# Kernel optimization log

Measured on AMD Instinct MI355X. Metric: run time of the kernel, lower is better.

## Reference

```python
import jax, jax.numpy as jnp
import numpy as np
import math

N_HEADS = 16
D_MODEL = 1024
M = D_MODEL // N_HEADS  # per-head dim = 64

def _kaiming_uniform(key, shape):
    # torch kaiming_uniform_ with a=sqrt(5) on [h, fan_in, fan_out]-style 3D tensor:
    # fan_in = shape[1] (size of dim 1), gain = sqrt(2/(1+a^2)) = sqrt(1/3)
    fan_in = shape[1]
    gain = math.sqrt(2.0 / (1.0 + 5.0))
    bound = gain * math.sqrt(3.0 / fan_in)
    return jax.random.uniform(key, shape, dtype=jnp.float32, minval=-bound, maxval=bound)

def setup_inputs() -> dict:
    key = jax.random.key(0)
    kx, kq, kk, kv, ko = jax.random.split(key, 5)
    x = jax.random.normal(kx, (4, 2048, D_MODEL), dtype=jnp.float32)
    W_q = _kaiming_uniform(kq, (N_HEADS, D_MODEL, M))
    W_k = _kaiming_uniform(kk, (N_HEADS, D_MODEL, M))
    W_v = _kaiming_uniform(kv, (N_HEADS, D_MODEL, M))
    W_o = _kaiming_uniform(ko, (N_HEADS, M, D_MODEL))
    return {"x": x, "W_q": W_q, "W_k": W_k, "W_v": W_v, "W_o": W_o}

def reference(x, W_q, W_k, W_v, W_o):
    # x: [b, s, d]; W_q/W_k/W_v: [h, d, m]; W_o: [h, m, d]
    q = jnp.einsum('bsd,hdm->bhsm', x, W_q)
    k = jnp.einsum('bsd,hdm->bhsm', x, W_k)
    v = jnp.einsum('bsd,hdm->bhsm', x, W_v)
    scale = 1.0 / math.sqrt(q.shape[-1])
    scores = jnp.einsum('bhsm,bhtm->bhst', q, k) * scale  # [b,h,s,s]
    attn = jax.nn.softmax(scores, axis=-1)
    ctx = jnp.einsum('bhst,bhtm->bhsm', attn, v)
    out = jnp.einsum('bhsm,hmd->bsd', ctx, W_o)  # sum over heads
    return out
```

## Files before the change

kernel.cpp:

```cpp
#include <hip/hip_runtime.h>
#include <hip/hip_bf16.h>

typedef __attribute__((ext_vector_type(8))) short short8;
typedef __attribute__((ext_vector_type(8))) _Float16 half8;
typedef __attribute__((ext_vector_type(4))) float f32x4;
typedef __attribute__((ext_vector_type(16))) float f32x16;
typedef __attribute__((ext_vector_type(4))) unsigned int uint4v;
typedef __attribute__((ext_vector_type(2))) unsigned int uint2v;

#define NB 4
#define NH 16
#define NS 2048
#define ND 1024
#define NM 64
#define R_TOT 8192
#define N_QKV 3072
#define QKV_ONE 8388608
#define SCALE_Q 0.18033688011112042f

static __device__ __forceinline__ unsigned short f2h(float f) {
    _Float16 h = (_Float16)f;
    return __builtin_bit_cast(unsigned short, h);
}
static __device__ __forceinline__ unsigned cvtpk_h(float lo, float hiv) {
    unsigned r;
    asm("v_cvt_pkrtz_f16_f32 %0, %1, %2" : "=v"(r) : "v"(lo), "v"(hiv));
    return r;
}
static __device__ __forceinline__ void gl_lds16(const unsigned short* g, unsigned short* l) {
    __builtin_amdgcn_global_load_lds((const __attribute__((address_space(1))) void*)g,
                                     (__attribute__((address_space(3))) void*)l, 16, 0, 0);
}
static __device__ __forceinline__ half8 rd_swz(const unsigned short* base, int row, int col) {
    int byte = (row << 7) + (col << 1);
    byte ^= (row & 7) << 4;
    return *(const half8*)((const char*)base + byte);
}

__global__ __launch_bounds__(256) void k_convert_x(const float* __restrict__ x,
                                                   unsigned short* __restrict__ xh) {
    int i = blockIdx.x * 256 + threadIdx.x;
    const float4* xp = (const float4*)x;
    float4 v = xp[i];
    ushort4 o;
    o.x = f2h(v.x); o.y = f2h(v.y); o.z = f2h(v.z); o.w = f2h(v.w);
    ((ushort4*)xh)[i] = o;
}

__global__ __launch_bounds__(256) void k_convert_wqkv(const float* __restrict__ Wq,
                                                      const float* __restrict__ Wk,
                                                      const float* __restrict__ Wv,
                                                      unsigned short* __restrict__ BT) {
    int i = blockIdx.x * 256 + threadIdx.x;
    int d = i & 1023;
    int n = i >> 10;
    int w = n >> 10;
    int h = (n >> 6) & 15;
    int m = n & 63;
    const float* W = (w == 0) ? Wq : ((w == 1) ? Wk : Wv);
    float v = W[((size_t)h * ND + d) * NM + m];
    if (w == 0) v *= SCALE_Q;
    BT[i] = f2h(v);
}

__global__ __launch_bounds__(256) void k_convert_wo(const float* __restrict__ Wo,
                                                    unsigned short* __restrict__ BTo) {
    int i = blockIdx.x * 256 + threadIdx.x;
    int n = i & 1023;
    int d = i >> 10;
    BTo[i] = f2h(Wo[(size_t)n * ND + d]);
}

#define QBM 256
#define QBN 192
__global__ __launch_bounds__(512, 2) void k_gemm_qkv(const unsigned short* __restrict__ A,
                                                     const unsigned short* __restrict__ BT,
                                                     unsigned short* __restrict__ qkv) {
    __shared__ unsigned short L[2][(QBM + QBN) * 64];
    int tid = threadIdx.x;
    int bx = blockIdx.x;
    int swz = (bx & 7) * 64 + (bx >> 3);
    int rt = swz & 31;
    int ct = swz >> 5;
    int r0 = rt * QBM, c0 = ct * QBN;
    int lane = tid & 63, wid = tid >> 6;
    int l15 = lane & 15, grp = lane >> 4;
    int wrow = (wid >> 2) * 128;
    int wcol = (wid & 3) * 48;

    f32x4 acc[8][3] = {};

    auto stageA = [&](int bufi, int k0) {
        #pragma unroll
        for (int r = 0; r < 4; ++r) {
            int off = r * 4096 + tid * 8;
            int row = off >> 6;
            int sch = ((off >> 3) & 7) ^ (row & 7);
            gl_lds16(A + (size_t)(r0 + row) * 1024 + k0 + sch * 8, &L[bufi][off]);
        }
    };
    auto stageB = [&](int bufi, int k0) {
        #pragma unroll
        for (int r = 0; r < 3; ++r) {
            int off = r * 4096 + tid * 8;
            int row = off >> 6;
            int sch = ((off >> 3) & 7) ^ (row & 7);
            gl_lds16(BT + (size_t)(c0 + row) * 1024 + k0 + sch * 8, &L[bufi][QBM * 64 + off]);
        }
    };

    stageA(0, 0);
    stageB(0, 0);
    asm volatile("s_waitcnt vmcnt(0)" ::: "memory");
    __builtin_amdgcn_s_barrier();

    for (int t = 0; t < 16; ++t) {
        int buf = t & 1;
        const unsigned short* As = L[buf];
        const unsigned short* Bs = L[buf] + QBM * 64;

        half8 af[8], bf[3];
        #pragma unroll
        for (int i = 0; i < 8; ++i) af[i] = rd_swz(As, wrow + i * 16 + l15, grp * 8);
        #pragma unroll
        for (int j = 0; j < 3; ++j) bf[j] = rd_swz(Bs, wcol + j * 16 + l15, grp * 8);
        if (t < 15) { stageA(buf ^ 1, (t + 1) * 64); stageB(buf ^ 1, (t + 1) * 64); }
        __builtin_amdgcn_sched_barrier(0);
        __builtin_amdgcn_s_setprio(1);
        #pragma unroll
        for (int i = 0; i < 8; ++i)
            #pragma unroll
            for (int j = 0; j < 3; ++j)
                acc[i][j] = __builtin_amdgcn_mfma_f32_16x16x32_f16(af[i], bf[j], acc[i][j], 0, 0, 0);
        __builtin_amdgcn_s_setprio(0);

        #pragma unroll
        for (int i = 0; i < 8; ++i) af[i] = rd_swz(As, wrow + i * 16 + l15, 32 + grp * 8);
        #pragma unroll
        for (int j = 0; j < 3; ++j) bf[j] = rd_swz(Bs, wcol + j * 16 + l15, 32 + grp * 8);
        __builtin_amdgcn_s_setprio(1);
        #pragma unroll
        for (int i = 0; i < 8; ++i)
            #pragma unroll
            for (int j = 0; j < 3; ++j)
                acc[i][j] = __builtin_amdgcn_mfma_f32_16x16x32_f16(af[i], bf[j], acc[i][j], 0, 0, 0);
        __builtin_amdgcn_s_setprio(0);

        asm volatile("s_waitcnt vmcnt(0)" ::: "memory");
        __builtin_amdgcn_s_barrier();
    }

    #pragma unroll
    for (int j = 0; j < 3; ++j) {
        int n_base = c0 + wcol + j * 16;
        int w = n_base >> 10;
        int nh = n_base + l15;
        int h = (nh >> 6) & 15;
        int m = nh & 63;
        if (w == 2) {
            unsigned short* outp = qkv + 2 * (size_t)QKV_ONE;
            #pragma unroll
            for (int i = 0; i < 8; ++i) {
                int rb = r0 + wrow + i * 16 + grp * 4;
                int bb = rb >> 11, s = rb & 2047;
                ushort4 pv;
                pv.x = f2h(acc[i][j][0]);
                pv.y = f2h(acc[i][j][1]);
                pv.z = f2h(acc[i][j][2]);
                pv.w = f2h(acc[i][j][3]);
                *(ushort4*)(outp + ((size_t)(bb * NH + h) * NM + m) * NS + s) = pv;
            }
        } else {
            unsigned short* outp = qkv + (size_t)w * QKV_ONE;
            #pragma unroll
            for (int i = 0; i < 8; ++i) {
                int rb = r0 + wrow + i * 16 + grp * 4;
                #pragma unroll
                for (int reg = 0; reg < 4; ++reg) {
                    int r = rb + reg;
                    int bb = r >> 11, s = r & 2047;
                    outp[((size_t)(bb * NH + h) * NS + s) * NM + m] = f2h(acc[i][j][reg]);
                }
            }
        }
    }
}

__global__ __launch_bounds__(512) void k_attn(const unsigned short* __restrict__ qkv,
                                              unsigned short* __restrict__ ctx) {
    __shared__ unsigned short Ks[2][4096];
    __shared__ unsigned short Vs[2][4096];

    int tid = threadIdx.x;
    int lane = tid & 63, wid = tid >> 6;
    int l31 = lane & 31, hi = lane >> 5;

    int bid = blockIdx.x;
    int xcd = bid & 7;
    int j = bid >> 3;
    int bh = xcd * 8 + (j >> 3);
    int qb = j & 7;
    int b = bh >> 4, h = bh & 15;

    size_t hb = (size_t)bh * NS * NM;
    const unsigned short* Qg = qkv + hb;
    const unsigned short* Kg = qkv + QKV_ONE + hb;
    const unsigned short* Vt = qkv + 2 * (size_t)QKV_ONE + hb;

    int q0 = qb * 256 + wid * 32;

    half8 qf[4];
    #pragma unroll
    for (int kk = 0; kk < 4; ++kk)
        qf[kk] = *(const half8*)(Qg + (size_t)(q0 + l31) * NM + kk * 16 + hi * 8);

    half8 ones;
    #pragma unroll
    for (int e = 0; e < 8; ++e) ones[e] = (_Float16)1.0f;

    f32x16 accO0 = {}, accO1 = {}, accS = {};

    const unsigned short* gsrc0;
    const unsigned short* gsrc1;
    unsigned short* lbase0;
    unsigned short* lbase1;
    int step0, step1;
    {
        int seg = wid * 2;
        int off = (seg & 7) * 512 + lane * 8;
        int row = off >> 6;
        int sch = ((off >> 3) & 7) ^ (row & 7);
        if (seg < 8) { gsrc0 = Kg + row * NM + sch * 8; step0 = NM;  lbase0 = &Ks[0][off]; }
        else         { gsrc0 = Vt + (size_t)row * NS + sch * 8; step0 = 1; lbase0 = &Vs[0][off]; }
        seg = wid * 2 + 1;
        off = (seg & 7) * 512 + lane * 8;
        row = off >> 6;
        sch = ((off >> 3) & 7) ^ (row & 7);
        if (seg < 8) { gsrc1 = Kg + row * NM + sch * 8; step1 = NM;  lbase1 = &Ks[0][off]; }
        else         { gsrc1 = Vt + (size_t)row * NS + sch * 8; step1 = 1; lbase1 = &Vs[0][off]; }
    }
    auto stage = [&](int bufi, int t0) {
        gl_lds16(gsrc0 + (size_t)t0 * step0, lbase0 + bufi * 4096);
        gl_lds16(gsrc1 + (size_t)t0 * step1, lbase1 + bufi * 4096);
    };

    stage(0, 0);
    stage(1, 64);

    for (int t = 0; t < 32; ++t) {
        int buf = t & 1;
        if (t < 31) asm volatile("s_waitcnt vmcnt(2)" ::: "memory");
        else        asm volatile("s_waitcnt vmcnt(0)" ::: "memory");
        __builtin_amdgcn_s_barrier();
        __builtin_amdgcn_sched_barrier(0);
        const unsigned short* Kb = Ks[buf];
        const unsigned short* Vb = Vs[buf];

        f32x16 s0v = {}, s1v = {};
        __builtin_amdgcn_s_setprio(1);
        #pragma unroll
        for (int kk = 0; kk < 4; ++kk) {
            int col = kk * 16 + hi * 8;
            s0v = __builtin_amdgcn_mfma_f32_32x32x16_f16(rd_swz(Kb, l31, col), qf[kk], s0v, 0, 0, 0);
            s1v = __builtin_amdgcn_mfma_f32_32x32x16_f16(rd_swz(Kb, 32 + l31, col), qf[kk], s1v, 0, 0, 0);
        }
        __builtin_amdgcn_s_setprio(0);

        unsigned pk0[8], pk1[8];
        #pragma unroll
        for (int jj = 0; jj < 8; ++jj) {
            float a0 = __builtin_amdgcn_exp2f(s0v[2 * jj]);
            float b0 = __builtin_amdgcn_exp2f(s0v[2 * jj + 1]);
            float a1 = __builtin_amdgcn_exp2f(s1v[2 * jj]);
            float b1 = __builtin_amdgcn_exp2f(s1v[2 * jj + 1]);
            pk0[jj] = cvtpk_h(a0, b0);
            pk1[jj] = cvtpk_h(a1, b1);
        }

        __builtin_amdgcn_s_setprio(1);
        #pragma unroll
        for (int kt = 0; kt < 4; ++kt) {
            unsigned w0, w1, w2, w3;
            if (kt < 2) {
                int base = (kt & 1) * 4;
                w0 = pk0[base + 0]; w1 = pk0[base + 1];
                w2 = pk0[base + 2]; w3 = pk0[base + 3];
            } else {
                int base = (kt & 1) * 4;
                w0 = pk1[base + 0]; w1 = pk1[base + 1];
                w2 = pk1[base + 2]; w3 = pk1[base + 3];
            }
            uint2v r02 = __builtin_amdgcn_permlane32_swap(w0, w2, false, false);
            uint2v r13 = __builtin_amdgcn_permlane32_swap(w1, w3, false, false);
            uint4v av;
            av[0] = r02[0]; av[1] = r13[0]; av[2] = r02[1]; av[3] = r13[1];
            half8 af = __builtin_bit_cast(half8, av);
            int col = kt * 16 + hi * 8;
            accO0 = __builtin_amdgcn_mfma_f32_32x32x16_f16(af, rd_swz(Vb, l31, col), accO0, 0, 0, 0);
            accO1 = __builtin_amdgcn_mfma_f32_32x32x16_f16(af, rd_swz(Vb, 32 + l31, col), accO1, 0, 0, 0);
            accS  = __builtin_amdgcn_mfma_f32_32x32x16_f16(af, ones, accS, 0, 0, 0);
        }
        __builtin_amdgcn_s_setprio(0);

        __builtin_amdgcn_sched_barrier(0);
        __builtin_amdgcn_s_barrier();
        if (t < 30) stage(buf, (t + 2) * 64);
    }

    #pragma unroll
    for (int reg = 0; reg < 16; ++reg) {
        int q = (reg & 3) + 8 * (reg >> 2) + 4 * hi;
        float linv = 1.0f / accS[reg];
        size_t ob = ((size_t)b * NS + (q0 + q)) * ND + h * 64 + l31;
        ctx[ob] = f2h(accO0[reg] * linv);
        ctx[ob + 32] = f2h(accO1[reg] * linv);
    }
}

__global__ __launch_bounds__(256) void k_gemm_out(const unsigned short* __restrict__ A,
                                                  const unsigned short* __restrict__ BT,
                                                  float* __restrict__ Cf) {
    __shared__ unsigned short As[128 * 64];
    __shared__ unsigned short Bs[128 * 64];
    int tid = threadIdx.x;
    int bx = blockIdx.x;
    int rt = bx & 63, ct = bx >> 6;
    int r0 = rt * 128, c0 = ct * 128;
    int lane = tid & 63, wid = tid >> 6;
    int l15 = lane & 15, grp = lane >> 4;
    int wr = (wid >> 1) * 64, wc = (wid & 1) * 64;
    f32x4 acc[4][4] = {};

    for (int k0 = 0; k0 < 1024; k0 += 64) {
        #pragma unroll
        for (int i = 0; i < 4; ++i) {
            int seg = wid * 4 + i;
            int row = seg * 8 + (lane >> 3);
            int sch = (lane & 7) ^ (row & 7);
            gl_lds16(A + (size_t)(r0 + row) * 1024 + k0 + sch * 8, As + seg * 512 + lane * 8);
            gl_lds16(BT + (size_t)(c0 + row) * 1024 + k0 + sch * 8, Bs + seg * 512 + lane * 8);
        }
        __syncthreads();
        #pragma unroll
        for (int ks = 0; ks < 64; ks += 32) {
            half8 af[4], bf[4];
            #pragma unroll
            for (int i = 0; i < 4; ++i)
                af[i] = rd_swz(As, wr + i * 16 + l15, ks + grp * 8);
            #pragma unroll
            for (int j = 0; j < 4; ++j)
                bf[j] = rd_swz(Bs, wc + j * 16 + l15, ks + grp * 8);
            #pragma unroll
            for (int i = 0; i < 4; ++i)
                #pragma unroll
                for (int j = 0; j < 4; ++j)
                    acc[i][j] = __builtin_amdgcn_mfma_f32_16x16x32_f16(af[i], bf[j], acc[i][j], 0, 0, 0);
        }
        __syncthreads();
    }
    #pragma unroll
    for (int i = 0; i < 4; ++i)
        #pragma unroll
        for (int j = 0; j < 4; ++j)
            #pragma unroll
            for (int reg = 0; reg < 4; ++reg) {
                int r = r0 + wr + i * 16 + grp * 4 + reg;
                int c = c0 + wc + j * 16 + l15;
                Cf[(size_t)r * 1024 + c] = acc[i][j][reg];
            }
}

extern "C" void kernel_launch(void* const* d_in, const int* in_sizes, int n_in,
                              void* d_out, int out_size, void* d_ws, size_t ws_size,
                              hipStream_t stream) {
    (void)in_sizes; (void)n_in; (void)out_size; (void)ws_size;
    const float* x  = (const float*)d_in[0];
    const float* Wq = (const float*)d_in[1];
    const float* Wk = (const float*)d_in[2];
    const float* Wv = (const float*)d_in[3];
    const float* Wo = (const float*)d_in[4];

    char* ws = (char*)d_ws;
    unsigned short* Xh   = (unsigned short*)ws;  ws += (size_t)R_TOT * 1024 * 2;
    unsigned short* BTq  = (unsigned short*)ws;  ws += (size_t)N_QKV * 1024 * 2;
    unsigned short* BTo  = (unsigned short*)ws;  ws += (size_t)1024 * 1024 * 2;
    unsigned short* QKV  = (unsigned short*)ws;  ws += (size_t)3 * QKV_ONE * 2;
    unsigned short* Ctx  = (unsigned short*)ws;  ws += (size_t)R_TOT * 1024 * 2;

    k_convert_x<<<dim3(R_TOT * 1024 / 4 / 256), dim3(256), 0, stream>>>(x, Xh);
    k_convert_wqkv<<<dim3(N_QKV * 1024 / 256), dim3(256), 0, stream>>>(Wq, Wk, Wv, BTq);
    k_convert_wo<<<dim3(1024 * 1024 / 256), dim3(256), 0, stream>>>(Wo, BTo);
    k_gemm_qkv<<<dim3(512), dim3(512), 0, stream>>>(Xh, BTq, QKV);
    k_attn<<<dim3(512), dim3(512), 0, stream>>>(QKV, Ctx);
    k_gemm_out<<<dim3(64 * 8), dim3(256), 0, stream>>>(Ctx, BTo, (float*)d_out);
}
```

Before: 193.0 us.

## Restructure output GEMM with larger tiles and double-buffered LDS prefetch

Rewrites the output projection GEMM to use 256x128 tiles with 512 threads, double-buffered LDS so the next K-slice loads while MFMAs run, and a block-index swizzle for L2 locality. It also adds s_setprio around MFMA bursts. The aim is to hide global-load latency and cut the number of barrier stalls per K step. In exchange it uses 96KB of LDS per block and launches only 256 blocks, which may underfill 256 CUs.

```diff
diff --git a/kernel.cpp b/kernel.cpp
--- a/kernel.cpp
+++ b/kernel.cpp
@@ -317,55 +317,93 @@
     }
 }
 
-__global__ __launch_bounds__(256) void k_gemm_out(const unsigned short* __restrict__ A,
-                                                  const unsigned short* __restrict__ BT,
-                                                  float* __restrict__ Cf) {
-    __shared__ unsigned short As[128 * 64];
-    __shared__ unsigned short Bs[128 * 64];
+#define OBM 256
+#define OBN 128
+__global__ __launch_bounds__(512, 2) void k_gemm_out(const unsigned short* __restrict__ A,
+                                                     const unsigned short* __restrict__ BT,
+                                                     float* __restrict__ Cf) {
+    __shared__ unsigned short L[2][(OBM + OBN) * 64];
     int tid = threadIdx.x;
     int bx = blockIdx.x;
-    int rt = bx & 63, ct = bx >> 6;
-    int r0 = rt * 128, c0 = ct * 128;
+    int swz = (bx & 7) * 32 + (bx >> 3);
+    int rt = swz & 31;
+    int ct = swz >> 5;
+    int r0 = rt * OBM, c0 = ct * OBN;
     int lane = tid & 63, wid = tid >> 6;
     int l15 = lane & 15, grp = lane >> 4;
-    int wr = (wid >> 1) * 64, wc = (wid & 1) * 64;
-    f32x4 acc[4][4] = {};
-
-    for (int k0 = 0; k0 < 1024; k0 += 64) {
-        #pragma unroll
-        for (int i = 0; i < 4; ++i) {
-            int seg = wid * 4 + i;
-            int row = seg * 8 + (lane >> 3);
-            int sch = (lane & 7) ^ (row & 7);
-            gl_lds16(A + (size_t)(r0 + row) * 1024 + k0 + sch * 8, As + seg * 512 + lane * 8);
-            gl_lds16(BT + (size_t)(c0 + row) * 1024 + k0 + sch * 8, Bs + seg * 512 + lane * 8);
-        }
-        __syncthreads();
-        #pragma unroll
-        for (int ks = 0; ks < 64; ks += 32) {
-            half8 af[4], bf[4];
-            #pragma unroll
-            for (int i = 0; i < 4; ++i)
-                af[i] = rd_swz(As, wr + i * 16 + l15, ks + grp * 8);
-            #pragma unroll
-            for (int j = 0; j < 4; ++j)
-                bf[j] = rd_swz(Bs, wc + j * 16 + l15, ks + grp * 8);
-            #pragma unroll
-            for (int i = 0; i < 4; ++i)
-                #pragma unroll
-                for (int j = 0; j < 4; ++j)
-                    acc[i][j] = __builtin_amdgcn_mfma_f32_16x16x32_f16(af[i], bf[j], acc[i][j], 0, 0, 0);
-        }
-        __syncthreads();
-    }
+    int wrow = (wid >> 2) * 128;
+    int wcol = (wid & 3) * 32;
+
+    f32x4 acc[8][2] = {};
+
+    auto stageA = [&](int bufi, int k0) {
+        #pragma unroll
+        for (int r = 0; r < 4; ++r) {
+            int off = r * 4096 + tid * 8;
+            int row = off >> 6;
+            int sch = ((off >> 3) & 7) ^ (row & 7);
+            gl_lds16(A + (size_t)(r0 + row) * 1024 + k0 + sch * 8, &L[bufi][off]);
+        }
+    };
+    auto stageB = [&](int bufi, int k0) {
+        #pragma unroll
+        for (int r = 0; r < 2; ++r) {
+            int off = r * 4096 + tid * 8;
+            int row = off >> 6;
+            int sch = ((off >> 3) & 7) ^ (row & 7);
+            gl_lds16(BT + (size_t)(c0 + row) * 1024 + k0 + sch * 8, &L[bufi][OBM * 64 + off]);
+        }
+    };
+
+    stageA(0, 0);
+    stageB(0, 0);
+    asm volatile("s_waitcnt vmcnt(0)" ::: "memory");
+    __builtin_amdgcn_s_barrier();
+
+    for (int t = 0; t < 16; ++t) {
+        int buf = t & 1;
+        const unsigned short* As = L[buf];
+        const unsigned short* Bs = L[buf] + OBM * 64;
+
+        half8 af[8], bf[2];
+        #pragma unroll
+        for (int i = 0; i < 8; ++i) af[i] = rd_swz(As, wrow + i * 16 + l15, grp * 8);
+        #pragma unroll
+        for (int j = 0; j < 2; ++j) bf[j] = rd_swz(Bs, wcol + j * 16 + l15, grp * 8);
+        if (t < 15) { stageA(buf ^ 1, (t + 1) * 64); stageB(buf ^ 1, (t + 1) * 64); }
+        __builtin_amdgcn_sched_barrier(0);
+        __builtin_amdgcn_s_setprio(1);
+        #pragma unroll
+        for (int i = 0; i < 8; ++i)
+            #pragma unroll
+            for (int j = 0; j < 2; ++j)
+                acc[i][j] = __builtin_amdgcn_mfma_f32_16x16x32_f16(af[i], bf[j], acc[i][j], 0, 0, 0);
+        __builtin_amdgcn_s_setprio(0);
+
+        #pragma unroll
+        for (int i = 0; i < 8; ++i) af[i] = rd_swz(As, wrow + i * 16 + l15, 32 + grp * 8);
+        #pragma unroll
+        for (int j = 0; j < 2; ++j) bf[j] = rd_swz(Bs, wcol + j * 16 + l15, 32 + grp * 8);
+        __builtin_amdgcn_s_setprio(1);
+        #pragma unroll
+        for (int i = 0; i < 8; ++i)
+            #pragma unroll
+            for (int j = 0; j < 2; ++j)
+                acc[i][j] = __builtin_amdgcn_mfma_f32_16x16x32_f16(af[i], bf[j], acc[i][j], 0, 0, 0);
+        __builtin_amdgcn_s_setprio(0);
+
+        asm volatile("s_waitcnt vmcnt(0)" ::: "memory");
+        __builtin_amdgcn_s_barrier();
+    }
+
     #pragma unroll
-    for (int i = 0; i < 4; ++i)
-        #pragma unroll
-        for (int j = 0; j < 4; ++j)
+    for (int i = 0; i < 8; ++i)
+        #pragma unroll
+        for (int j = 0; j < 2; ++j)
             #pragma unroll
             for (int reg = 0; reg < 4; ++reg) {
-                int r = r0 + wr + i * 16 + grp * 4 + reg;
-                int c = c0 + wc + j * 16 + l15;
+                int r = r0 + wrow + i * 16 + grp * 4 + reg;
+                int c = c0 + wcol + j * 16 + l15;
                 Cf[(size_t)r * 1024 + c] = acc[i][j][reg];
             }
 }
@@ -392,5 +430,5 @@
     k_convert_wo<<<dim3(1024 * 1024 / 256), dim3(256), 0, stream>>>(Wo, BTo);
     k_gemm_qkv<<<dim3(512), dim3(512), 0, stream>>>(Xh, BTq, QKV);
     k_attn<<<dim3(512), dim3(512), 0, stream>>>(QKV, Ctx);
-    k_gemm_out<<<dim3(64 * 8), dim3(256), 0, stream>>>(Ctx, BTo, (float*)d_out);
-}
+    k_gemm_out<<<dim3(256), dim3(512), 0, stream>>>(Ctx, BTo, (float*)d_out);
+}
```

New measurement: 194.9 us. No clear change (+1.0%).
